# Performance work log

Hardware: AMD Instinct MI355X
Metric: run time of the kernel (lower is better)

Reference implementation:

```python
import jax, jax.numpy as jnp
import numpy as np

MAX_DISP = 4  # matches init_kwargs


def setup_inputs() -> dict:
    key = jax.random.key(0)
    k1, k2 = jax.random.split(key)
    x_1 = jax.random.normal(k1, (8, 64, 256, 256), dtype=jnp.float32)
    x_2 = jax.random.normal(k2, (8, 64, 256, 256), dtype=jnp.float32)
    return {"x_1": x_1, "x_2": x_2}


def reference(x_1, x_2):
    md = MAX_DISP
    B, C, H, W = x_1.shape
    # zero-pad x_2 spatially by max_disp on all sides
    x2p = jnp.pad(x_2, ((0, 0), (0, 0), (md, md), (md, md)))
    D = 2 * md + 1
    # row-major over (dx, dy), matching torch.meshgrid(indexing='ij')
    outs = [
        jnp.mean(x_1 * jax.lax.dynamic_slice(x2p, (0, 0, dx, dy), (B, C, H, W)),
                 axis=1, keepdims=True)
        for dx in range(D) for dy in range(D)
    ]
    return jnp.concatenate(outs, axis=1)  # [B, D*D, H, W]
```

## Files before the change

kernel.cpp:

```cpp
#include <hip/hip_runtime.h>


namespace {
constexpr int kB = 8;
constexpr int kC = 64;
constexpr int kH = 256;
constexpr int kW = 256;
constexpr int kD = 9;
constexpr int kMD = 4;
}

__global__ __launch_bounds__(64) void corr_kernel(
    const float* __restrict__ x1, const float* __restrict__ x2,
    float* __restrict__ out) {
  const int bx = blockIdx.x;
  const int dx = bx % kD;
  const int h  = (bx / kD) % kH;
  const int b  = bx / (kD * kH);
  const int row = h + dx - kMD;
  const int w0  = (int)threadIdx.x * 4;

  float acc[kD][4];
#pragma unroll
  for (int dy = 0; dy < kD; ++dy)
#pragma unroll
    for (int j = 0; j < 4; ++j) acc[dy][j] = 0.0f;

  if (row >= 0 && row < kH) {
    const float* p1 = x1 + ((size_t)(b * kC) * kH + h) * kW + w0;
    const float* p2 = x2 + ((size_t)(b * kC) * kH + row) * kW + w0;
    const bool hasL = (w0 >= 4);
    const bool hasR = (w0 + 7 < kW);
    for (int c = 0; c < kC; ++c) {
      const float4 a  = *reinterpret_cast<const float4*>(p1);
      const float4 tB = *reinterpret_cast<const float4*>(p2);
      float4 tA = make_float4(0.f, 0.f, 0.f, 0.f);
      float4 tC = make_float4(0.f, 0.f, 0.f, 0.f);
      if (hasL) tA = *reinterpret_cast<const float4*>(p2 - 4);
      if (hasR) tC = *reinterpret_cast<const float4*>(p2 + 4);

      const float av[4] = {a.x, a.y, a.z, a.w};
      const float t[12] = {tA.x, tA.y, tA.z, tA.w,
                           tB.x, tB.y, tB.z, tB.w,
                           tC.x, tC.y, tC.z, tC.w};
#pragma unroll
      for (int dy = 0; dy < kD; ++dy)
#pragma unroll
        for (int j = 0; j < 4; ++j)
          acc[dy][j] = fmaf(av[j], t[dy + j], acc[dy][j]);

      p1 += kH * kW;
      p2 += kH * kW;
    }
  }

  const float inv = 1.0f / (float)kC;
  float* po = out + (((size_t)b * (kD * kD) + dx * kD) * kH + h) * kW + w0;
#pragma unroll
  for (int dy = 0; dy < kD; ++dy) {
    float4 o = make_float4(acc[dy][0] * inv, acc[dy][1] * inv,
                           acc[dy][2] * inv, acc[dy][3] * inv);
    *reinterpret_cast<float4*>(po) = o;
    po += (size_t)kH * kW;
  }
}

extern "C" void kernel_launch(void* const* d_in, const int* in_sizes, int n_in,
                              void* d_out, int out_size, void* d_ws, size_t ws_size,
                              hipStream_t stream) {
  const float* x1 = (const float*)d_in[0];
  const float* x2 = (const float*)d_in[1];
  float* out = (float*)d_out;
  const int grid = kB * kH * kD;
  corr_kernel<<<grid, 64, 0, stream>>>(x1, x2, out);
}
```

Before: 225.4 us.

## Rewrite correlation as bf16 MFMA kernel with LDS staging of shifted tiles

Replaces the per-(row,dx) scalar FMA kernel with a 256-thread block per (batch,row,64-column quarter). The block stages x1 and a 9-row halo of x2 in LDS as packed bf16 and computes the channel dot products with 16x16x32 bf16 MFMA, extracting the band diagonal for the 9 dy offsets. Results go through LDS and are written out as coalesced float4 stores. This trades fp32 accuracy for bf16 inputs and wastes most MFMA output lanes on off-band entries, but cuts redundant global loads of x2 across dx.

```diff
diff --git a/kernel.cpp b/kernel.cpp
--- a/kernel.cpp
+++ b/kernel.cpp
@@ -1,67 +1,141 @@
 #include <hip/hip_runtime.h>
+#include <hip/hip_bf16.h>
 
 
 namespace {
-constexpr int kB = 8;
-constexpr int kC = 64;
-constexpr int kH = 256;
-constexpr int kW = 256;
-constexpr int kD = 9;
-constexpr int kMD = 4;
+constexpr int kC  = 64;
+constexpr int kH  = 256;
+constexpr int kW  = 256;
+constexpr int kHW = kH * kW;
+constexpr int kD  = 9;
+constexpr int kX1Str  = 68;
+constexpr int kX2Str  = 84;
+constexpr int kX2Blk  = 16 * kX2Str;
+constexpr int kX2Base = 16 * kX1Str;
+constexpr int kLdsDw  = kX2Base + kD * kX2Blk;
 }
 
-__global__ __launch_bounds__(64) void corr_kernel(
+using short8 = __attribute__((ext_vector_type(8))) short;
+using f32x4  = __attribute__((ext_vector_type(4))) float;
+
+__device__ __forceinline__ unsigned pkbf(float lo, float hi) {
+  const unsigned short a =
+      __builtin_bit_cast(unsigned short, __float2bfloat16(lo));
+  const unsigned short b =
+      __builtin_bit_cast(unsigned short, __float2bfloat16(hi));
+  return (unsigned)a | ((unsigned)b << 16);
+}
+
+__global__ __launch_bounds__(256) void corr_mfma(
     const float* __restrict__ x1, const float* __restrict__ x2,
     float* __restrict__ out) {
-  const int bx = blockIdx.x;
-  const int dx = bx % kD;
-  const int h  = (bx / kD) % kH;
-  const int b  = bx / (kD * kH);
-  const int row = h + dx - kMD;
-  const int w0  = (int)threadIdx.x * 4;
+  __shared__ __attribute__((aligned(16))) unsigned lds[kLdsDw];
+  float* ldsf = (float*)lds;
 
-  float acc[kD][4];
+  const int b    = blockIdx.x & 7;
+  const int slot = blockIdx.x >> 3;
+  const int h    = slot >> 2;
+  const int wq   = slot & 3;
+  const int w0   = wq * 64;
+
+  const int tid  = (int)threadIdx.x;
+  const int wv   = tid >> 6;
+  const int lane = tid & 63;
+  const int lg   = lane >> 4;
+  const int ln   = lane & 15;
+
+  f32x4 acc[kD][2];
 #pragma unroll
-  for (int dy = 0; dy < kD; ++dy)
+  for (int dx = 0; dx < kD; ++dx)
 #pragma unroll
-    for (int j = 0; j < 4; ++j) acc[dy][j] = 0.0f;
+    for (int qt = 0; qt < 2; ++qt) acc[dx][qt] = (f32x4)0.0f;
 
-  if (row >= 0 && row < kH) {
-    const float* p1 = x1 + ((size_t)(b * kC) * kH + h) * kW + w0;
-    const float* p2 = x2 + ((size_t)(b * kC) * kH + row) * kW + w0;
-    const bool hasL = (w0 >= 4);
-    const bool hasR = (w0 + 7 < kW);
-    for (int c = 0; c < kC; ++c) {
-      const float4 a  = *reinterpret_cast<const float4*>(p1);
-      const float4 tB = *reinterpret_cast<const float4*>(p2);
-      float4 tA = make_float4(0.f, 0.f, 0.f, 0.f);
-      float4 tC = make_float4(0.f, 0.f, 0.f, 0.f);
-      if (hasL) tA = *reinterpret_cast<const float4*>(p2 - 4);
-      if (hasR) tC = *reinterpret_cast<const float4*>(p2 + 4);
+  const int p1 = tid >> 4, w41 = tid & 15;
 
-      const float av[4] = {a.x, a.y, a.z, a.w};
-      const float t[12] = {tA.x, tA.y, tA.z, tA.w,
-                           tB.x, tB.y, tB.z, tB.w,
-                           tC.x, tC.y, tC.z, tC.w};
+#pragma unroll 1
+  for (int pass = 0; pass < 2; ++pass) {
+    const int c0 = pass * 32;
+
+    {
+      const float* s1 =
+          x1 + ((size_t)(b * kC + c0 + 2 * p1) * kH + h) * kW + w0 + 4 * w41;
+      const float4 v0 = *(const float4*)s1;
+      const float4 v1 = *(const float4*)(s1 + kHW);
+      uint4 q;
+      q.x = pkbf(v0.x, v1.x); q.y = pkbf(v0.y, v1.y);
+      q.z = pkbf(v0.z, v1.z); q.w = pkbf(v0.w, v1.w);
+      *(uint4*)&lds[p1 * kX1Str + 4 * w41] = q;
+    }
+#pragma unroll 1
+    for (int i = 0; i < 12; ++i) {
+      const int s = tid + 256 * i;
+      if (s < 2880) {
+        const int w4 = s % 20;
+        const int rest = s / 20;
+        const int p = rest & 15;
+        const int r = rest >> 4;
+        const int g = h + r - 4;
+        const int w = w0 - 4 + 4 * w4;
+        uint4 q = make_uint4(0u, 0u, 0u, 0u);
+        if (g >= 0 && g < kH && w >= 0 && w <= kW - 4) {
+          const float* s2 =
+              x2 + ((size_t)(b * kC + c0 + 2 * p) * kH + g) * kW + w;
+          const float4 v0 = *(const float4*)s2;
+          const float4 v1 = *(const float4*)(s2 + kHW);
+          q.x = pkbf(v0.x, v1.x); q.y = pkbf(v0.y, v1.y);
+          q.z = pkbf(v0.z, v1.z); q.w = pkbf(v0.w, v1.w);
+        }
+        *(uint4*)&lds[kX2Base + r * kX2Blk + p * kX2Str + 4 * w4] = q;
+      }
+    }
+    __syncthreads();
+
+    union Frag { unsigned u[4]; short8 s; };
+    Frag fa;
 #pragma unroll
-      for (int dy = 0; dy < kD; ++dy)
+    for (int r = 0; r < 4; ++r)
+      fa.u[r] = lds[(lg * 4 + r) * kX1Str + wv * 16 + ln];
+
 #pragma unroll
-        for (int j = 0; j < 4; ++j)
-          acc[dy][j] = fmaf(av[j], t[dy + j], acc[dy][j]);
-
-      p1 += kH * kW;
-      p2 += kH * kW;
+    for (int dx = 0; dx < kD; ++dx) {
+      const int rb = kX2Base + dx * kX2Blk;
+#pragma unroll
+      for (int qt = 0; qt < 2; ++qt) {
+        const int qb = wv * 16 + qt * 16 + ln;
+        Frag fb;
+#pragma unroll
+        for (int r = 0; r < 4; ++r)
+          fb.u[r] = lds[rb + (lg * 4 + r) * kX2Str + qb];
+        acc[dx][qt] = __builtin_amdgcn_mfma_f32_16x16x32_bf16(
+            fa.s, fb.s, acc[dx][qt], 0, 0, 0);
+      }
     }
+    __syncthreads();
   }
 
-  const float inv = 1.0f / (float)kC;
-  float* po = out + (((size_t)b * (kD * kD) + dx * kD) * kH + h) * kW + w0;
+  const float inv = 1.0f / 64.0f;
 #pragma unroll
-  for (int dy = 0; dy < kD; ++dy) {
-    float4 o = make_float4(acc[dy][0] * inv, acc[dy][1] * inv,
-                           acc[dy][2] * inv, acc[dy][3] * inv);
-    *reinterpret_cast<float4*>(po) = o;
-    po += (size_t)kH * kW;
+  for (int dx = 0; dx < kD; ++dx)
+#pragma unroll
+    for (int r = 0; r < 4; ++r) {
+      const int m = lg * 4 + r;
+      const int dyL = ln - m;
+      if (dyL >= 0 && dyL <= 8)
+        ldsf[(dx * 9 + dyL) * 68 + wv * 16 + m] = acc[dx][0][r] * inv;
+      const int dyR = ln - m + 16;
+      if (dyR <= 8)
+        ldsf[(dx * 9 + dyR) * 68 + wv * 16 + m] = acc[dx][1][r] * inv;
+    }
+  __syncthreads();
+
+#pragma unroll
+  for (int i = 0; i < 6; ++i) {
+    const int s = tid + 256 * i;
+    if (s < 81 * 16) {
+      const int dd = s >> 4, w4 = s & 15;
+      const float4 v = *(const float4*)&ldsf[dd * 68 + 4 * w4];
+      *(float4*)(out + (((size_t)b * 81 + dd) * kH + h) * kW + w0 + 4 * w4) = v;
+    }
   }
 }
 
@@ -71,6 +145,6 @@
   const float* x1 = (const float*)d_in[0];
   const float* x2 = (const float*)d_in[1];
   float* out = (float*)d_out;
-  const int grid = kB * kH * kD;
-  corr_kernel<<<grid, 64, 0, stream>>>(x1, x2, out);
+  const int grid = 8 * kH * 4;
+  corr_mfma<<<grid, 256, 0, stream>>>(x1, x2, out);
 }
```

Result: slower. 379.5 us (+68.4%).
